# Kernel tuning notes

Hardware: AMD Instinct MI355X
Metric: run time of the kernel (lower is better)

Reference implementation:

```python
import jax, jax.numpy as jnp
import numpy as np

EMBED_DIM = 1024
N_HEADS = 16
HEAD_DIM = EMBED_DIM // N_HEADS
BATCH = 2
SEQ = 2048


def setup_inputs() -> dict:
    key = jax.random.key(0)
    ks = jax.random.split(key, 12)
    s = 1.0 / np.sqrt(EMBED_DIM)
    return {
        "x": jax.random.normal(ks[0], (BATCH, SEQ, EMBED_DIM), jnp.float32),
        "q_w": jax.random.normal(ks[1], (EMBED_DIM, EMBED_DIM), jnp.float32) * s,
        "q_b": jax.random.normal(ks[2], (EMBED_DIM,), jnp.float32) * s,
        "k_w": jax.random.normal(ks[3], (EMBED_DIM, EMBED_DIM), jnp.float32) * s,
        "k_b": jax.random.normal(ks[4], (EMBED_DIM,), jnp.float32) * s,
        "v_w": jax.random.normal(ks[5], (EMBED_DIM, EMBED_DIM), jnp.float32) * s,
        "v_b": jax.random.normal(ks[6], (EMBED_DIM,), jnp.float32) * s,
        "phase": jax.random.normal(ks[7], (N_HEADS, HEAD_DIM), jnp.float32),
        "entanglement": jax.random.normal(ks[8], (N_HEADS, HEAD_DIM, HEAD_DIM), jnp.float32) * 0.1,
        "out_w": jax.random.normal(ks[9], (EMBED_DIM, EMBED_DIM), jnp.float32) * s,
        "out_b": jax.random.normal(ks[10], (EMBED_DIM,), jnp.float32) * s,
    }


def reference(x, q_w, q_b, k_w, k_b, v_w, v_b, phase, entanglement, out_w, out_b):
    b, s, _ = x.shape
    # projections -> [b, h, s, d]
    def split_heads(y):
        return y.reshape(b, s, N_HEADS, HEAD_DIM).transpose(0, 2, 1, 3)
    Q = split_heads(x @ q_w + q_b)
    K = split_heads(x @ k_w + k_b)
    V = split_heads(x @ v_w + v_b)
    # real part of phase-rotated Q/K: Q * cos(phase) (imag discarded by .real)
    cosp = jnp.cos(phase)[None, :, None, :]  # [1, h, 1, d]
    Qc = Q * cosp
    Kc = K * cosp
    scores = jnp.einsum('bhqd,bhkd->bhqk', Qc, Kc) / np.sqrt(HEAD_DIM)
    # bilinear entanglement term: Q . E . K^T per head
    scores = scores + jnp.einsum('bhqd,hde,bhke->bhqk', Q, entanglement, K)
    attn = jax.nn.softmax(scores, axis=-1)
    attended = jnp.einsum('bhqk,bhkd->bhqd', attn, V)
    attended = attended.transpose(0, 2, 1, 3).reshape(b, s, EMBED_DIM)
    return attended @ out_w + out_b
```

## Files before the change

### kernel.cpp

```cpp
#include <hip/hip_runtime.h>
#include <hip/hip_bf16.h>

typedef __bf16 bf16;
typedef __bf16 bf16x8 __attribute__((ext_vector_type(8)));
typedef __bf16 bf16x4 __attribute__((ext_vector_type(4)));
typedef float f32x4 __attribute__((ext_vector_type(4)));
typedef float f32x16 __attribute__((ext_vector_type(16)));
typedef unsigned int u32x2 __attribute__((ext_vector_type(2)));

#define EMBED 1024
#define NH 16
#define HD 64
#define BATCH 2
#define SEQ 2048
#define MTOK 4096
#define LOG2E 1.4426950408889634f

static __device__ __forceinline__ float fast_exp2(float x) {
#if __has_builtin(__builtin_amdgcn_exp2f)
  return __builtin_amdgcn_exp2f(x);
#else
  float r;
  asm("v_exp_f32 %0, %1" : "=v"(r) : "v"(x));
  return r;
#endif
}

static __device__ __forceinline__ f32x4 mfma16(bf16x8 a, bf16x8 b, f32x4 c) {
  return __builtin_amdgcn_mfma_f32_16x16x32_bf16(a, b, c, 0, 0, 0);
}
static __device__ __forceinline__ f32x16 mfma32(bf16x8 a, bf16x8 b, f32x16 c) {
  return __builtin_amdgcn_mfma_f32_32x32x16_bf16(a, b, c, 0, 0, 0);
}

static __device__ __forceinline__ void gld_lds16(const bf16* g, bf16* l) {
  __builtin_amdgcn_global_load_lds(
      (const __attribute__((address_space(1))) void*)g,
      (__attribute__((address_space(3))) void*)l, 16, 0, 0);
}

__global__ __launch_bounds__(256) void prep_kernel(
    const float* __restrict__ x, const float* __restrict__ qw,
    const float* __restrict__ qb, const float* __restrict__ kw,
    const float* __restrict__ vw, const float* __restrict__ ow,
    const float* __restrict__ ent, const float* __restrict__ phase,
    bf16* __restrict__ xb, bf16* __restrict__ wtall, bf16* __restrict__ wot,
    float* __restrict__ beff) {
  __shared__ float t0[64][65];
  __shared__ float t1[64][65];
  const int bb = blockIdx.x;
  const int tid = threadIdx.x;

  if (bb < 2048) {
    const int n4 = MTOK * EMBED / 4;
    int i = bb * 256 + tid;
    for (; i < n4; i += 2048 * 256) {
      f32x4 v = ((const f32x4*)x)[i];
      bf16x4 o;
      o[0] = (bf16)v[0]; o[1] = (bf16)v[1]; o[2] = (bf16)v[2]; o[3] = (bf16)v[3];
      ((bf16x4*)xb)[i] = o;
    }
    return;
  }
  if (bb < 2816) {
    const int idx = (bb - 2048) & 255;
    const float* W = (bb < 2304) ? kw : (bb < 2560) ? vw : ow;
    bf16* Wt = (bb < 2304) ? (wtall + 1024 * 1024)
             : (bb < 2560) ? (wtall + 2 * 1024 * 1024) : wot;
    const int bc = (idx & 15) * 64;
    const int br = (idx >> 4) * 64;
#pragma unroll
    for (int j = 0; j < 16; j++) {
      int id2 = j * 256 + tid;
      int r = id2 >> 6, c = id2 & 63;
      t0[r][c] = W[(size_t)(br + r) * EMBED + bc + c];
    }
    __syncthreads();
#pragma unroll
    for (int j = 0; j < 16; j++) {
      int id2 = j * 256 + tid;
      int r = id2 >> 6, c = id2 & 63;
      Wt[(size_t)(bc + r) * EMBED + br + c] = (bf16)t0[c][r];
    }
    return;
  }
  if (bb < 3072) {
    const int idx = bb - 2816;
    const int h = idx >> 4;
    const int ibase = (idx & 15) * 64;
#pragma unroll
    for (int j = 0; j < 16; j++) {
      int id2 = j * 256 + tid;
      int i = id2 >> 6, d = id2 & 63;
      t0[i][d] = qw[(size_t)(ibase + i) * EMBED + h * HD + d];
    }
#pragma unroll
    for (int j = 0; j < 16; j++) {
      int id2 = j * 256 + tid;
      int d = id2 >> 6, e = id2 & 63;
      float v = ent[((size_t)h * HD + d) * HD + e];
      if (d == e) { float cp = cosf(phase[h * HD + d]); v += cp * cp * 0.125f; }
      t1[d][e] = v * LOG2E;
    }
    __syncthreads();
    const int i = tid & 63;
    const int e0 = (tid >> 6) * 16;
    float s[16];
#pragma unroll
    for (int ee = 0; ee < 16; ee++) s[ee] = 0.f;
    for (int d = 0; d < 64; d++) {
      float qv = t0[i][d];
#pragma unroll
      for (int ee = 0; ee < 16; ee++) s[ee] += qv * t1[d][e0 + ee];
    }
#pragma unroll
    for (int ee = 0; ee < 16; ee++)
      wtall[(size_t)(h * HD + e0 + ee) * EMBED + ibase + i] = (bf16)s[ee];
    return;
  }
  const int h = bb - 3072;
  if (tid < 64) {
    const int e = tid;
    float s = 0.f;
    for (int d = 0; d < 64; d++) {
      float v = ent[((size_t)h * HD + d) * HD + e];
      if (d == e) { float cp = cosf(phase[h * HD + d]); v += cp * cp * 0.125f; }
      s += qb[h * HD + d] * v;
    }
    beff[h * HD + e] = s * LOG2E;
  }
}

template <int EPI>
__global__ __launch_bounds__(256) void gemm_bt_kernel(
    const bf16* __restrict__ A, const bf16* __restrict__ Bt,
    const float* __restrict__ bias_q, const float* __restrict__ bias_k,
    const float* __restrict__ bias_v, const float* __restrict__ bias_o,
    bf16* __restrict__ Qp, bf16* __restrict__ Kp, bf16* __restrict__ Vt,
    float* __restrict__ Fout) {
  const int tid = threadIdx.x;
  const int lane = tid & 63, w = tid >> 6;
  const int g = lane >> 4, r15 = lane & 15;
  const int wr = w >> 1, wc = w & 1;
  const int bm = blockIdx.x * 128;
  const int bn = blockIdx.y * 128;

  __shared__ bf16 sA[128 * 32];
  __shared__ bf16 sB[128 * 32];

  f32x4 acc[4][4];
#pragma unroll
  for (int m = 0; m < 4; m++)
#pragma unroll
    for (int n = 0; n < 4; n++) acc[m][n] = (f32x4){0.f, 0.f, 0.f, 0.f};

  const int srow = tid >> 2;
  const int scol = (tid & 3) << 3;
  const bf16* aptr = A + (size_t)(bm + srow) * EMBED + scol;
  const bf16* bptr = Bt + (size_t)(bn + srow) * EMBED + scol;
  bf16* la = sA + tid * 8;
  bf16* lb = sB + tid * 8;

  for (int k0 = 0; k0 < EMBED; k0 += 32) {
    __syncthreads();
    gld_lds16(aptr + k0, la);
    gld_lds16(aptr + k0 + 64 * EMBED, la + 64 * 32);
    gld_lds16(bptr + k0, lb);
    gld_lds16(bptr + k0 + 64 * EMBED, lb + 64 * 32);
    __syncthreads();
    bf16x8 af[4], bfv[4];
#pragma unroll
    for (int m = 0; m < 4; m++)
      af[m] = *(const bf16x8*)&sA[(wr * 64 + m * 16 + r15) * 32 + g * 8];
#pragma unroll
    for (int n = 0; n < 4; n++)
      bfv[n] = *(const bf16x8*)&sB[(wc * 64 + n * 16 + r15) * 32 + g * 8];
#pragma unroll
    for (int m = 0; m < 4; m++)
#pragma unroll
      for (int n = 0; n < 4; n++) acc[m][n] = mfma16(af[m], bfv[n], acc[m][n]);
  }

  const int orow0 = bm + wr * 64;
  if (EPI == 0) {
    const int seg = bn >> 10;
    const int clb = (bn & 1023) + wc * 64;
#pragma unroll
    for (int n = 0; n < 4; n++) {
      const int cl = clb + n * 16 + r15;
      const float bias = (seg == 0) ? bias_q[cl] : (seg == 1) ? bias_k[cl] : bias_v[cl];
#pragma unroll
      for (int m = 0; m < 4; m++) {
        const int row0 = orow0 + m * 16 + g * 4;
        if (seg == 2) {
          const int b = row0 >> 11, s = row0 & 2047;
          const int hh = cl >> 6, d = cl & 63;
          bf16x4 pk;
#pragma unroll
          for (int r = 0; r < 4; r++) pk[r] = (bf16)(acc[m][n][r] + bias);
          *(bf16x4*)(Vt + ((size_t)((b * NH + hh) * HD + d)) * SEQ + s) = pk;
        } else {
          bf16* dst = ((seg == 0) ? Qp : Kp) + (size_t)row0 * EMBED + cl;
#pragma unroll
          for (int r = 0; r < 4; r++) dst[(size_t)r * EMBED] = (bf16)(acc[m][n][r] + bias);
        }
      }
    }
  } else {
    const int ocol0 = bn + wc * 64;
#pragma unroll
    for (int n = 0; n < 4; n++) {
      const int col = ocol0 + n * 16 + r15;
      const float bias = bias_o[col];
#pragma unroll
      for (int m = 0; m < 4; m++) {
        const int row0 = orow0 + m * 16 + g * 4;
#pragma unroll
        for (int r = 0; r < 4; r++)
          Fout[(size_t)(row0 + r) * EMBED + col] = acc[m][n][r] + bias;
      }
    }
  }
}

__global__ __launch_bounds__(256, 2) void flash_attn_kernel(
    const bf16* __restrict__ Qp, const bf16* __restrict__ Kp,
    const bf16* __restrict__ Vt, bf16* __restrict__ Op) {
  const int tid = threadIdx.x, lane = tid & 63, w = tid >> 6;
  const int q31 = lane & 31, hi = lane >> 5;
  const int flat = blockIdx.x;
  const int c = (flat & 7) * 64 + (flat >> 3);
  const int bh = c >> 4, qt = c & 15;
  const int b = bh >> 4, h = bh & 15;

  __shared__ bf16 sK[2][8192];
  __shared__ bf16 sV[2][8192];

  const int strow = tid >> 3;
  const int stsb = ((tid & 7) << 4) ^ ((strow & 7) << 4);
  const int svrow = tid >> 4;
  const int svsb = ((tid & 15) << 4) ^ ((svrow & 7) << 4);

  const char* kgbase = (const char*)(Kp + ((size_t)b * SEQ) * EMBED + h * HD);
  const char* vgbase = (const char*)(Vt + (size_t)bh * HD * SEQ);

  auto stage = [&](int buf, int kv0) {
#pragma unroll
    for (int i = 0; i < 4; i++) {
      const int row = i * 32 + strow;
      gld_lds16((const bf16*)(kgbase + (size_t)(kv0 + row) * (EMBED * 2) + stsb),
                &sK[buf][i * 2048 + tid * 8]);
    }
#pragma unroll
    for (int i = 0; i < 4; i++) {
      const int row = i * 16 + svrow;
      gld_lds16((const bf16*)(vgbase + (size_t)row * (SEQ * 2) + (size_t)kv0 * 2 + svsb),
                &sV[buf][i * 2048 + tid * 8]);
    }
  };

  stage(0, 0);

  const int qbase = qt * 128 + w * 32;
  const int qrow = qbase + q31;
  const bf16* qptr = Qp + ((size_t)(b * SEQ + qrow)) * EMBED + h * HD;
  bf16x8 aq[4];
#pragma unroll
  for (int ds = 0; ds < 4; ds++)
    aq[ds] = *(const bf16x8*)(qptr + ds * 16 + hi * 8);

  const int sz = (q31 & 7) << 4;
  int cofs[4];
#pragma unroll
  for (int i = 0; i < 4; i++) cofs[i] = ((i * 32 + hi * 16) ^ sz);
  int vofs[8];
#pragma unroll
  for (int i = 0; i < 8; i++) vofs[i] = ((i * 32 + hi * 16) ^ sz);

  f32x16 o0, o1;
#pragma unroll
  for (int i = 0; i < 16; i++) { o0[i] = 0.f; o1[i] = 0.f; }
  float mrow = -3.0e38f, lrow = 0.f;

  for (int it = 0; it < SEQ / 128; ++it) {
    const int cur = it & 1;
    if (it + 1 < SEQ / 128) {
      stage(cur ^ 1, (it + 1) * 128);
      asm volatile("s_waitcnt vmcnt(8)" ::: "memory");
    } else {
      asm volatile("s_waitcnt vmcnt(0)" ::: "memory");
    }
    __builtin_amdgcn_s_barrier();

    const char* kc = (const char*)&sK[cur][0] + q31 * 128;
    const char* vc = (const char*)&sV[cur][0] + q31 * 256;

    f32x16 s0, s1, s2, s3;
#pragma unroll
    for (int i = 0; i < 16; i++) { s0[i] = 0.f; s1[i] = 0.f; s2[i] = 0.f; s3[i] = 0.f; }
    __builtin_amdgcn_s_setprio(1);
#pragma unroll
    for (int ds = 0; ds < 4; ds++) {
      bf16x8 bk0 = *(const bf16x8*)(kc + cofs[ds]);
      bf16x8 bk1 = *(const bf16x8*)(kc + 4096 + cofs[ds]);
      bf16x8 bk2 = *(const bf16x8*)(kc + 8192 + cofs[ds]);
      bf16x8 bk3 = *(const bf16x8*)(kc + 12288 + cofs[ds]);
      s0 = mfma32(bk0, aq[ds], s0);
      s1 = mfma32(bk1, aq[ds], s1);
      s2 = mfma32(bk2, aq[ds], s2);
      s3 = mfma32(bk3, aq[ds], s3);
    }
    __builtin_amdgcn_s_setprio(0);

    float mt = s0[0];
#pragma unroll
    for (int i = 1; i < 16; i++) mt = fmaxf(mt, s0[i]);
#pragma unroll
    for (int i = 0; i < 16; i++) mt = fmaxf(mt, fmaxf(s1[i], fmaxf(s2[i], s3[i])));
    {
      u32x2 sm = __builtin_amdgcn_permlane32_swap(__float_as_uint(mt),
                                                  __float_as_uint(mt), false, false);
      mt = fmaxf(__uint_as_float(sm.x), __uint_as_float(sm.y));
    }
    if (__any(mt > mrow + 8.f)) {
      const float mn = fmaxf(mrow, mt);
      const float al = fast_exp2(mrow - mn);
      mrow = mn;
      lrow *= al;
      o0 *= al;
      o1 *= al;
    }

    union B4 { bf16x4 v; unsigned int u[2]; };
    B4 qd[16];
    float lsum = 0.f;
#pragma unroll
    for (int j = 0; j < 4; j++)
#pragma unroll
      for (int r = 0; r < 4; r++) {
        float pv = fast_exp2(s0[4 * j + r] - mrow);
        lsum += pv; qd[j].v[r] = (bf16)pv;
      }
#pragma unroll
    for (int j = 0; j < 4; j++)
#pragma unroll
      for (int r = 0; r < 4; r++) {
        float pv = fast_exp2(s1[4 * j + r] - mrow);
        lsum += pv; qd[4 + j].v[r] = (bf16)pv;
      }
#pragma unroll
    for (int j = 0; j < 4; j++)
#pragma unroll
      for (int r = 0; r < 4; r++) {
        float pv = fast_exp2(s2[4 * j + r] - mrow);
        lsum += pv; qd[8 + j].v[r] = (bf16)pv;
      }
#pragma unroll
    for (int j = 0; j < 4; j++)
#pragma unroll
      for (int r = 0; r < 4; r++) {
        float pv = fast_exp2(s3[4 * j + r] - mrow);
        lsum += pv; qd[12 + j].v[r] = (bf16)pv;
      }
    {
      u32x2 ss = __builtin_amdgcn_permlane32_swap(__float_as_uint(lsum),
                                                  __float_as_uint(lsum), false, false);
      lrow += __uint_as_float(ss.x) + __uint_as_float(ss.y);
    }

    bf16x8 pfrag[8];
#pragma unroll
    for (int kt = 0; kt < 8; kt++) {
      u32x2 p0 = __builtin_amdgcn_permlane32_swap(qd[2 * kt].u[0],
                                                  qd[2 * kt + 1].u[0], false, false);
      u32x2 p1 = __builtin_amdgcn_permlane32_swap(qd[2 * kt].u[1],
                                                  qd[2 * kt + 1].u[1], false, false);
      union { unsigned int u[4]; bf16x8 v; } f;
      f.u[0] = p0.x; f.u[1] = p1.x; f.u[2] = p0.y; f.u[3] = p1.y;
      pfrag[kt] = f.v;
    }

    __builtin_amdgcn_s_setprio(1);
#pragma unroll
    for (int kt = 0; kt < 8; kt++) {
      bf16x8 av0 = *(const bf16x8*)(vc + vofs[kt]);
      bf16x8 av1 = *(const bf16x8*)(vc + 8192 + vofs[kt]);
      o0 = mfma32(av0, pfrag[kt], o0);
      o1 = mfma32(av1, pfrag[kt], o1);
    }
    __builtin_amdgcn_s_setprio(0);
    __builtin_amdgcn_s_barrier();
  }

  const float inv = 1.f / lrow;
  bf16* obase = Op + ((size_t)(b * SEQ + qrow)) * EMBED + h * HD;
#pragma unroll
  for (int j = 0; j < 4; j++) {
    bf16x4 st;
#pragma unroll
    for (int r = 0; r < 4; r++) st[r] = (bf16)(o0[4 * j + r] * inv);
    *(bf16x4*)(obase + 8 * j + 4 * hi) = st;
  }
#pragma unroll
  for (int j = 0; j < 4; j++) {
    bf16x4 st;
#pragma unroll
    for (int r = 0; r < 4; r++) st[r] = (bf16)(o1[4 * j + r] * inv);
    *(bf16x4*)(obase + 32 + 8 * j + 4 * hi) = st;
  }
}

extern "C" void kernel_launch(void* const* d_in, const int* in_sizes, int n_in,
                              void* d_out, int out_size, void* d_ws, size_t ws_size,
                              hipStream_t stream) {
  const float* x     = (const float*)d_in[0];
  const float* q_w   = (const float*)d_in[1];
  const float* q_b   = (const float*)d_in[2];
  const float* k_w   = (const float*)d_in[3];
  const float* k_b   = (const float*)d_in[4];
  const float* v_w   = (const float*)d_in[5];
  const float* v_b   = (const float*)d_in[6];
  const float* phase = (const float*)d_in[7];
  const float* ent   = (const float*)d_in[8];
  const float* out_w = (const float*)d_in[9];
  const float* out_b = (const float*)d_in[10];
  float* out = (float*)d_out;

  char* ws = (char*)d_ws;
  bf16* xb    = (bf16*)(ws + 0);
  bf16* wtall = (bf16*)(ws + 8388608);
  bf16* wot   = (bf16*)(ws + 14680064);
  float* beff = (float*)(ws + 16777216);
  bf16* Qp    = (bf16*)(ws + 16781312);
  bf16* Kp    = (bf16*)(ws + 25169920);
  bf16* Vt    = (bf16*)(ws + 33558528);
  (void)in_sizes; (void)n_in; (void)out_size; (void)ws_size;

  prep_kernel<<<3088, 256, 0, stream>>>(x, q_w, q_b, k_w, v_w, out_w, ent, phase,
                                        xb, wtall, wot, beff);

  gemm_bt_kernel<0><<<dim3(32, 24), 256, 0, stream>>>(
      xb, wtall, beff, k_b, v_b, nullptr, Qp, Kp, Vt, nullptr);

  flash_attn_kernel<<<512, 256, 0, stream>>>(Qp, Kp, Vt, xb);

  gemm_bt_kernel<1><<<dim3(32, 8), 256, 0, stream>>>(
      xb, wot, nullptr, nullptr, nullptr, out_b, nullptr, nullptr, nullptr, out);
}
```

Before: 136.9 us.

## Split attention key tile into two independent online-softmax streams

```diff
diff --git a/kernel.cpp b/kernel.cpp
--- a/kernel.cpp
+++ b/kernel.cpp
@@ -277,10 +277,12 @@
 #pragma unroll
   for (int i = 0; i < 8; i++) vofs[i] = ((i * 32 + hi * 16) ^ sz);
 
-  f32x16 o0, o1;
-#pragma unroll
-  for (int i = 0; i < 16; i++) { o0[i] = 0.f; o1[i] = 0.f; }
-  float mrow = -3.0e38f, lrow = 0.f;
+  f32x16 oA0, oA1, oB0, oB1;
+#pragma unroll
+  for (int i = 0; i < 16; i++) { oA0[i] = 0.f; oA1[i] = 0.f; oB0[i] = 0.f; oB1[i] = 0.f; }
+  float mA = -3.0e38f, lA = 0.f, mB = -3.0e38f, lB = 0.f;
+
+  union B4 { bf16x4 v; unsigned int u[2]; };
 
   for (int it = 0; it < SEQ / 128; ++it) {
     const int cur = it & 1;
@@ -295,117 +297,174 @@
     const char* kc = (const char*)&sK[cur][0] + q31 * 128;
     const char* vc = (const char*)&sV[cur][0] + q31 * 256;
 
-    f32x16 s0, s1, s2, s3;
-#pragma unroll
-    for (int i = 0; i < 16; i++) { s0[i] = 0.f; s1[i] = 0.f; s2[i] = 0.f; s3[i] = 0.f; }
+    f32x16 a0, a1, b0, b1;
+#pragma unroll
+    for (int i = 0; i < 16; i++) { a0[i] = 0.f; a1[i] = 0.f; b0[i] = 0.f; b1[i] = 0.f; }
     __builtin_amdgcn_s_setprio(1);
 #pragma unroll
     for (int ds = 0; ds < 4; ds++) {
-      bf16x8 bk0 = *(const bf16x8*)(kc + cofs[ds]);
-      bf16x8 bk1 = *(const bf16x8*)(kc + 4096 + cofs[ds]);
-      bf16x8 bk2 = *(const bf16x8*)(kc + 8192 + cofs[ds]);
-      bf16x8 bk3 = *(const bf16x8*)(kc + 12288 + cofs[ds]);
-      s0 = mfma32(bk0, aq[ds], s0);
-      s1 = mfma32(bk1, aq[ds], s1);
-      s2 = mfma32(bk2, aq[ds], s2);
-      s3 = mfma32(bk3, aq[ds], s3);
+      bf16x8 k0 = *(const bf16x8*)(kc + cofs[ds]);
+      bf16x8 k1 = *(const bf16x8*)(kc + 4096 + cofs[ds]);
+      bf16x8 k2 = *(const bf16x8*)(kc + 8192 + cofs[ds]);
+      bf16x8 k3 = *(const bf16x8*)(kc + 12288 + cofs[ds]);
+      a0 = mfma32(k0, aq[ds], a0);
+      a1 = mfma32(k1, aq[ds], a1);
+      b0 = mfma32(k2, aq[ds], b0);
+      b1 = mfma32(k3, aq[ds], b1);
     }
     __builtin_amdgcn_s_setprio(0);
 
-    float mt = s0[0];
-#pragma unroll
-    for (int i = 1; i < 16; i++) mt = fmaxf(mt, s0[i]);
-#pragma unroll
-    for (int i = 0; i < 16; i++) mt = fmaxf(mt, fmaxf(s1[i], fmaxf(s2[i], s3[i])));
+    bf16x8 pfA[2], pfB[2];
     {
+      float t8[8];
+#pragma unroll
+      for (int j = 0; j < 8; j++)
+        t8[j] = fmaxf(fmaxf(a0[j], a0[j + 8]), fmaxf(a1[j], a1[j + 8]));
+      float mt = fmaxf(fmaxf(fmaxf(t8[0], t8[4]), fmaxf(t8[1], t8[5])),
+                       fmaxf(fmaxf(t8[2], t8[6]), fmaxf(t8[3], t8[7])));
       u32x2 sm = __builtin_amdgcn_permlane32_swap(__float_as_uint(mt),
                                                   __float_as_uint(mt), false, false);
       mt = fmaxf(__uint_as_float(sm.x), __uint_as_float(sm.y));
-    }
-    if (__any(mt > mrow + 8.f)) {
-      const float mn = fmaxf(mrow, mt);
-      const float al = fast_exp2(mrow - mn);
-      mrow = mn;
-      lrow *= al;
-      o0 *= al;
-      o1 *= al;
-    }
-
-    union B4 { bf16x4 v; unsigned int u[2]; };
-    B4 qd[16];
-    float lsum = 0.f;
-#pragma unroll
-    for (int j = 0; j < 4; j++)
-#pragma unroll
-      for (int r = 0; r < 4; r++) {
-        float pv = fast_exp2(s0[4 * j + r] - mrow);
-        lsum += pv; qd[j].v[r] = (bf16)pv;
-      }
-#pragma unroll
-    for (int j = 0; j < 4; j++)
-#pragma unroll
-      for (int r = 0; r < 4; r++) {
-        float pv = fast_exp2(s1[4 * j + r] - mrow);
-        lsum += pv; qd[4 + j].v[r] = (bf16)pv;
-      }
-#pragma unroll
-    for (int j = 0; j < 4; j++)
-#pragma unroll
-      for (int r = 0; r < 4; r++) {
-        float pv = fast_exp2(s2[4 * j + r] - mrow);
-        lsum += pv; qd[8 + j].v[r] = (bf16)pv;
-      }
-#pragma unroll
-    for (int j = 0; j < 4; j++)
-#pragma unroll
-      for (int r = 0; r < 4; r++) {
-        float pv = fast_exp2(s3[4 * j + r] - mrow);
-        lsum += pv; qd[12 + j].v[r] = (bf16)pv;
-      }
-    {
+      if (__any(mt > mA + 8.f)) {
+        const float mn = fmaxf(mA, mt);
+        const float al = fast_exp2(mA - mn);
+        mA = mn; lA *= al; oA0 *= al; oA1 *= al;
+      }
+      B4 qd[8];
+      float c0 = 0.f, c1 = 0.f, c2 = 0.f, c3 = 0.f;
+#pragma unroll
+      for (int j = 0; j < 4; j++) {
+        float p0 = fast_exp2(a0[4 * j] - mA);
+        float p1 = fast_exp2(a0[4 * j + 1] - mA);
+        float p2 = fast_exp2(a0[4 * j + 2] - mA);
+        float p3 = fast_exp2(a0[4 * j + 3] - mA);
+        c0 += p0; c1 += p1; c2 += p2; c3 += p3;
+        qd[j].v[0] = (bf16)p0; qd[j].v[1] = (bf16)p1;
+        qd[j].v[2] = (bf16)p2; qd[j].v[3] = (bf16)p3;
+      }
+#pragma unroll
+      for (int j = 0; j < 4; j++) {
+        float p0 = fast_exp2(a1[4 * j] - mA);
+        float p1 = fast_exp2(a1[4 * j + 1] - mA);
+        float p2 = fast_exp2(a1[4 * j + 2] - mA);
+        float p3 = fast_exp2(a1[4 * j + 3] - mA);
+        c0 += p0; c1 += p1; c2 += p2; c3 += p3;
+        qd[4 + j].v[0] = (bf16)p0; qd[4 + j].v[1] = (bf16)p1;
+        qd[4 + j].v[2] = (bf16)p2; qd[4 + j].v[3] = (bf16)p3;
+      }
+      float lsum = (c0 + c1) + (c2 + c3);
       u32x2 ss = __builtin_amdgcn_permlane32_swap(__float_as_uint(lsum),
                                                   __float_as_uint(lsum), false, false);
-      lrow += __uint_as_float(ss.x) + __uint_as_float(ss.y);
-    }
-
-    bf16x8 pfrag[8];
-#pragma unroll
-    for (int kt = 0; kt < 8; kt++) {
-      u32x2 p0 = __builtin_amdgcn_permlane32_swap(qd[2 * kt].u[0],
-                                                  qd[2 * kt + 1].u[0], false, false);
-      u32x2 p1 = __builtin_amdgcn_permlane32_swap(qd[2 * kt].u[1],
-                                                  qd[2 * kt + 1].u[1], false, false);
-      union { unsigned int u[4]; bf16x8 v; } f;
-      f.u[0] = p0.x; f.u[1] = p1.x; f.u[2] = p0.y; f.u[3] = p1.y;
-      pfrag[kt] = f.v;
-    }
-
-    __builtin_amdgcn_s_setprio(1);
-#pragma unroll
-    for (int kt = 0; kt < 8; kt++) {
-      bf16x8 av0 = *(const bf16x8*)(vc + vofs[kt]);
-      bf16x8 av1 = *(const bf16x8*)(vc + 8192 + vofs[kt]);
-      o0 = mfma32(av0, pfrag[kt], o0);
-      o1 = mfma32(av1, pfrag[kt], o1);
-    }
-    __builtin_amdgcn_s_setprio(0);
+      lA += __uint_as_float(ss.x) + __uint_as_float(ss.y);
+      bf16x8 pfrag[4];
+#pragma unroll
+      for (int kt = 0; kt < 4; kt++) {
+        u32x2 p0 = __builtin_amdgcn_permlane32_swap(qd[2 * kt].u[0],
+                                                    qd[2 * kt + 1].u[0], false, false);
+        u32x2 p1 = __builtin_amdgcn_permlane32_swap(qd[2 * kt].u[1],
+                                                    qd[2 * kt + 1].u[1], false, false);
+        union { unsigned int u[4]; bf16x8 v; } f;
+        f.u[0] = p0.x; f.u[1] = p1.x; f.u[2] = p0.y; f.u[3] = p1.y;
+        pfrag[kt] = f.v;
+      }
+      __builtin_amdgcn_s_setprio(1);
+#pragma unroll
+      for (int kt = 0; kt < 4; kt++) {
+        bf16x8 av0 = *(const bf16x8*)(vc + vofs[kt]);
+        bf16x8 av1 = *(const bf16x8*)(vc + 8192 + vofs[kt]);
+        oA0 = mfma32(av0, pfrag[kt], oA0);
+        oA1 = mfma32(av1, pfrag[kt], oA1);
+      }
+      __builtin_amdgcn_s_setprio(0);
+      (void)pfA;
+    }
+
+    {
+      float t8[8];
+#pragma unroll
+      for (int j = 0; j < 8; j++)
+        t8[j] = fmaxf(fmaxf(b0[j], b0[j + 8]), fmaxf(b1[j], b1[j + 8]));
+      float mt = fmaxf(fmaxf(fmaxf(t8[0], t8[4]), fmaxf(t8[1], t8[5])),
+                       fmaxf(fmaxf(t8[2], t8[6]), fmaxf(t8[3], t8[7])));
+      u32x2 sm = __builtin_amdgcn_permlane32_swap(__float_as_uint(mt),
+                                                  __float_as_uint(mt), false, false);
+      mt = fmaxf(__uint_as_float(sm.x), __uint_as_float(sm.y));
+      if (__any(mt > mB + 8.f)) {
+        const float mn = fmaxf(mB, mt);
+        const float al = fast_exp2(mB - mn);
+        mB = mn; lB *= al; oB0 *= al; oB1 *= al;
+      }
+      B4 qd[8];
+      float c0 = 0.f, c1 = 0.f, c2 = 0.f, c3 = 0.f;
+#pragma unroll
+      for (int j = 0; j < 4; j++) {
+        float p0 = fast_exp2(b0[4 * j] - mB);
+        float p1 = fast_exp2(b0[4 * j + 1] - mB);
+        float p2 = fast_exp2(b0[4 * j + 2] - mB);
+        float p3 = fast_exp2(b0[4 * j + 3] - mB);
+        c0 += p0; c1 += p1; c2 += p2; c3 += p3;
+        qd[j].v[0] = (bf16)p0; qd[j].v[1] = (bf16)p1;
+        qd[j].v[2] = (bf16)p2; qd[j].v[3] = (bf16)p3;
+      }
+#pragma unroll
+      for (int j = 0; j < 4; j++) {
+        float p0 = fast_exp2(b1[4 * j] - mB);
+        float p1 = fast_exp2(b1[4 * j + 1] - mB);
+        float p2 = fast_exp2(b1[4 * j + 2] - mB);
+        float p3 = fast_exp2(b1[4 * j + 3] - mB);
+        c0 += p0; c1 += p1; c2 += p2; c3 += p3;
+        qd[4 + j].v[0] = (bf16)p0; qd[4 + j].v[1] = (bf16)p1;
+        qd[4 + j].v[2] = (bf16)p2; qd[4 + j].v[3] = (bf16)p3;
+      }
+      float lsum = (c0 + c1) + (c2 + c3);
+      u32x2 ss = __builtin_amdgcn_permlane32_swap(__float_as_uint(lsum),
+                                                  __float_as_uint(lsum), false, false);
+      lB += __uint_as_float(ss.x) + __uint_as_float(ss.y);
+      bf16x8 pfrag[4];
+#pragma unroll
+      for (int kt = 0; kt < 4; kt++) {
+        u32x2 p0 = __builtin_amdgcn_permlane32_swap(qd[2 * kt].u[0],
+                                                    qd[2 * kt + 1].u[0], false, false);
+        u32x2 p1 = __builtin_amdgcn_permlane32_swap(qd[2 * kt].u[1],
+                                                    qd[2 * kt + 1].u[1], false, false);
+        union { unsigned int u[4]; bf16x8 v; } f;
+        f.u[0] = p0.x; f.u[1] = p1.x; f.u[2] = p0.y; f.u[3] = p1.y;
+        pfrag[kt] = f.v;
+      }
+      __builtin_amdgcn_s_setprio(1);
+#pragma unroll
+      for (int kt = 0; kt < 4; kt++) {
+        bf16x8 av0 = *(const bf16x8*)(vc + vofs[kt + 4]);
+        bf16x8 av1 = *(const bf16x8*)(vc + 8192 + vofs[kt + 4]);
+        oB0 = mfma32(av0, pfrag[kt], oB0);
+        oB1 = mfma32(av1, pfrag[kt], oB1);
+      }
+      __builtin_amdgcn_s_setprio(0);
+      (void)pfB;
+    }
     __builtin_amdgcn_s_barrier();
   }
 
-  const float inv = 1.f / lrow;
+  const float M = fmaxf(mA, mB);
+  const float wA = fast_exp2(mA - M), wB = fast_exp2(mB - M);
+  const float inv = 1.f / (lA * wA + lB * wB);
+  const float fA = wA * inv, fB = wB * inv;
+
   bf16* obase = Op + ((size_t)(b * SEQ + qrow)) * EMBED + h * HD;
 #pragma unroll
   for (int j = 0; j < 4; j++) {
     bf16x4 st;
 #pragma unroll
-    for (int r = 0; r < 4; r++) st[r] = (bf16)(o0[4 * j + r] * inv);
+    for (int r = 0; r < 4; r++)
+      st[r] = (bf16)(oA0[4 * j + r] * fA + oB0[4 * j + r] * fB);
     *(bf16x4*)(obase + 8 * j + 4 * hi) = st;
   }
 #pragma unroll
   for (int j = 0; j < 4; j++) {
     bf16x4 st;
 #pragma unroll
-    for (int r = 0; r < 4; r++) st[r] = (bf16)(o1[4 * j + r] * inv);
+    for (int r = 0; r < 4; r++)
+      st[r] = (bf16)(oA1[4 * j + r] * fA + oB1[4 * j + r] * fB);
     *(bf16x4*)(obase + 32 + 8 * j + 4 * hi) = st;
   }
 }
```

Measured after the change: 139.3 us. Within noise of the previous version (+1.7%).
